# Kernel optimization log

Hardware: AMD Instinct MI355X
Metric: run time of the kernel (lower is better)

The kernel has to match this reference:

```python
import jax, jax.numpy as jnp
import numpy as np

B, S, HID = 4, 2048, 1024
H, D = 16, 64  # num_attention_heads, attention_head_size


def setup_inputs() -> dict:
    key = jax.random.key(0)
    k1, k2, k3, k4 = jax.random.split(key, 4)
    scale = 0.02
    return {
        "hidden_states": jax.random.normal(k1, (B, S, HID), dtype=jnp.float32),
        "attention_mask": jnp.zeros((B, 1, 1, S), dtype=jnp.float32),
        "Wq": jax.random.normal(k2, (HID, HID), dtype=jnp.float32) * scale,
        "bq": jnp.zeros((HID,), dtype=jnp.float32),
        "Wk": jax.random.normal(k3, (HID, HID), dtype=jnp.float32) * scale,
        "bk": jnp.zeros((HID,), dtype=jnp.float32),
        "Wv": jax.random.normal(k4, (HID, HID), dtype=jnp.float32) * scale,
        "bv": jnp.zeros((HID,), dtype=jnp.float32),
    }


def _split_heads(x):
    # [B,S,HID] -> [B,H,S,D]
    b, s, _ = x.shape
    return x.reshape(b, s, H, D).transpose(0, 2, 1, 3)


def reference(hidden_states, attention_mask, Wq, bq, Wk, bk, Wv, bv):
    # nn.Linear applies x @ W.T + b
    q = _split_heads(hidden_states @ Wq.T + bq)  # [B,H,S,D]
    k = _split_heads(hidden_states @ Wk.T + bk)
    v = _split_heads(hidden_states @ Wv.T + bv)
    scores = jnp.einsum("bhqd,bhkd->bhqk", q, k) / jnp.sqrt(jnp.float32(D))
    scores = scores + attention_mask  # additive mask, broadcast [B,1,1,S]
    probs = jax.nn.softmax(scores, axis=-1)  # dropout prob = 0 -> identity
    ctx = jnp.einsum("bhqk,bhkd->bhqd", probs, v)  # [B,H,S,D]
    ctx = ctx.transpose(0, 2, 1, 3).reshape(hidden_states.shape[0], hidden_states.shape[1], HID)
    return ctx
```

## Files before the change

kernel.cpp:

```cpp
#include <hip/hip_runtime.h>
#include <stdint.h>

#define BB 4
#define SS 2048
#define HID 1024
#define NH 16
#define DH 64

using bf16x8 = __attribute__((ext_vector_type(8))) short;
using f32x4  = __attribute__((ext_vector_type(4))) float;

#define LOG2E 1.44269504088896340736f

__device__ __forceinline__ ushort f2bf(float f) {
  union { float f; uint32_t u; } v; v.f = f;
  return (ushort)((v.u + 0x7FFFu + ((v.u >> 16) & 1u)) >> 16);
}

__device__ __forceinline__ uint32_t cvt_pk_bf16(float a, float b) {
  uint32_t r;
  asm("v_cvt_pk_bf16_f32 %0, %1, %2" : "=v"(r) : "v"(a), "v"(b));
  return r;
}

__device__ __forceinline__ float exp2_hw(float x) {
  float r;
  asm("v_exp_f32 %0, %1" : "=v"(r) : "v"(x));
  return r;
}

__device__ __forceinline__ void gload_lds16(const ushort* g, ushort* l) {
  __builtin_amdgcn_global_load_lds(
      (const __attribute__((address_space(1))) uint32_t*)g,
      (__attribute__((address_space(3))) uint32_t*)l, 16, 0, 0);
}

__device__ __forceinline__ int vperm(int j) {
  return (j & 0x23) | ((j & 0x0C) << 1) | ((j & 0x10) >> 2);
}

__global__ void cvt_kernel(const float* __restrict__ x, const float* __restrict__ wq,
                           const float* __restrict__ wk, const float* __restrict__ wv,
                           const float* __restrict__ am,
                           ushort* __restrict__ xbf, ushort* __restrict__ wbf,
                           float* __restrict__ maskL) {
  const int64_t NX4 = (int64_t)BB * SS * HID / 4;
  const int64_t NW4 = (int64_t)HID * HID / 4;
  const int64_t NWT = 3 * NW4;
  int64_t i = (int64_t)blockIdx.x * blockDim.x + threadIdx.x;
  if (i >= NX4 + NWT) {
    const int64_t jm = i - (NX4 + NWT);
    float4 v = ((const float4*)am)[jm];
    v.x *= LOG2E; v.y *= LOG2E; v.z *= LOG2E; v.w *= LOG2E;
    ((float4*)maskL)[jm] = v;
    return;
  }
  float4 v;
  ushort4* dst;
  if (i < NX4) {
    v = ((const float4*)x)[i];
    dst = (ushort4*)xbf + i;
  } else {
    int64_t j = i - NX4;
    int w = (int)(j >> 18);
    int64_t k = j & (NW4 - 1);
    const float* src = (w == 0) ? wq : (w == 1) ? wk : wv;
    v = ((const float4*)src)[k];
    dst = (ushort4*)wbf + j;
  }
  ushort4 o;
  o.x = f2bf(v.x); o.y = f2bf(v.y); o.z = f2bf(v.z); o.w = f2bf(v.w);
  *dst = o;
}

__global__ __launch_bounds__(512, 2) void qkv_gemm(
    const ushort* __restrict__ xbf, const ushort* __restrict__ wbf,
    const float* __restrict__ bq, const float* __restrict__ bk,
    const float* __restrict__ bv,
    ushort* __restrict__ qws, ushort* __restrict__ kws, ushort* __restrict__ vtws) {
  __shared__ short Al[2][256][64];
  __shared__ short Bl[2][192][64];

  const int tid = threadIdx.x, wid = tid >> 6, lane = tid & 63;
  const int colL = lane & 15, rowg = lane >> 4;
  const int wr = wid >> 2, wc = wid & 3;

  const int wgid = (blockIdx.x & 7) * 64 + (blockIdx.x >> 3);
  const int m0 = (wgid >> 4) * 256;
  const int n0 = (wgid & 15) * 192;

  const int swzcol = (((tid & 7) * 16) ^ (((tid >> 3) & 7) << 4)) >> 1;
  const ushort* aSrc = xbf + (int64_t)(m0 + (tid >> 3)) * HID + swzcol;
  const ushort* bSrc = wbf + (int64_t)(n0 + (tid >> 3)) * HID + swzcol;
  ushort* Al_u = (ushort*)&Al[0][0][0];
  ushort* Bl_u = (ushort*)&Bl[0][0][0];

  auto stageA = [&](int kt, int r, int ps) {
    gload_lds16(aSrc + r * 64 * HID + kt * 64, Al_u + ps * 16384 + r * 4096 + wid * 512);
  };
  auto stageB = [&](int kt, int r, int ps) {
    gload_lds16(bSrc + r * 64 * HID + kt * 64, Bl_u + ps * 12288 + r * 4096 + wid * 512);
  };

  const int xsw = (colL & 7) << 4;
  const int offk0 = (rowg * 16) ^ xsw;
  const int offk1 = (64 + rowg * 16) ^ xsw;
  const int arow = (wr * 128 + colL) * 128;
  const int brow = (wc * 48 + colL) * 128;
  const char* AlC = (const char*)&Al[0][0][0];
  const char* BlC = (const char*)&Bl[0][0][0];

  f32x4 acc[8][3];
#pragma unroll
  for (int i = 0; i < 8; ++i)
#pragma unroll
    for (int j = 0; j < 3; ++j)
#pragma unroll
      for (int r = 0; r < 4; ++r) acc[i][j][r] = 0.f;

  stageB(0, 0, 0); stageB(0, 1, 0); stageB(0, 2, 0);
  stageA(0, 0, 0); stageA(0, 2, 0); stageA(0, 1, 0); stageA(0, 3, 0);
  asm volatile("s_waitcnt vmcnt(2)" ::: "memory");
  __builtin_amdgcn_s_barrier();

#define DO_PHASE(P, S1, S2, PRE_BAR2)                                          \
  {                                                                            \
    const int mfa = 2 * (P), mfb = 2 * (P) + 1;                                \
    bf16x8 aA0 = *(const bf16x8*)(kA0 + mfa * 2048);                           \
    bf16x8 aA1 = *(const bf16x8*)(kA1 + mfa * 2048);                           \
    bf16x8 aB0 = *(const bf16x8*)(kA0 + mfb * 2048);                           \
    bf16x8 aB1 = *(const bf16x8*)(kA1 + mfb * 2048);                           \
    S1; S2;                                                                    \
    __builtin_amdgcn_s_barrier();                                              \
    __builtin_amdgcn_s_setprio(1);                                             \
    _Pragma("unroll")                                                          \
    for (int nf = 0; nf < 3; ++nf) {                                           \
      acc[mfa][nf] = __builtin_amdgcn_mfma_f32_16x16x32_bf16(aA0, bfr[nf][0], acc[mfa][nf], 0, 0, 0); \
      acc[mfa][nf] = __builtin_amdgcn_mfma_f32_16x16x32_bf16(aA1, bfr[nf][1], acc[mfa][nf], 0, 0, 0); \
      acc[mfb][nf] = __builtin_amdgcn_mfma_f32_16x16x32_bf16(aB0, bfr[nf][0], acc[mfb][nf], 0, 0, 0); \
      acc[mfb][nf] = __builtin_amdgcn_mfma_f32_16x16x32_bf16(aB1, bfr[nf][1], acc[mfb][nf], 0, 0, 0); \
    }                                                                          \
    __builtin_amdgcn_s_setprio(0);                                             \
    PRE_BAR2;                                                                  \
    __builtin_amdgcn_s_barrier();                                              \
  }

  for (int t = 0; t < 16; ++t) {
    const int p = t & 1;
    const int ps = p ^ 1;
    const bool st = (t < 15);
    const int kt = t + 1;
    const char* kA0 = AlC + p * 32768 + arow + offk0;
    const char* kA1 = AlC + p * 32768 + arow + offk1;
    const char* kB0 = BlC + p * 24576 + brow + offk0;
    const char* kB1 = BlC + p * 24576 + brow + offk1;

    bf16x8 bfr[3][2];
#pragma unroll
    for (int nf = 0; nf < 3; ++nf) {
      bfr[nf][0] = *(const bf16x8*)(kB0 + nf * 2048);
      bfr[nf][1] = *(const bf16x8*)(kB1 + nf * 2048);
    }

    DO_PHASE(0, if (st) stageB(kt, 0, ps), if (st) stageB(kt, 1, ps), )
    DO_PHASE(1, if (st) stageB(kt, 2, ps), if (st) stageA(kt, 0, ps),
             if (t == 15) { asm volatile("s_waitcnt vmcnt(0)" ::: "memory"); }
             else        { asm volatile("s_waitcnt vmcnt(4)" ::: "memory"); })
    DO_PHASE(2, if (st) stageA(kt, 2, ps), if (st) stageA(kt, 1, ps), )
    DO_PHASE(3, if (st) stageA(kt, 3, ps), ,
             if (t == 14) { asm volatile("s_waitcnt vmcnt(0)" ::: "memory"); }
             else if (st) { asm volatile("s_waitcnt vmcnt(2)" ::: "memory"); })
  }
#undef DO_PHASE

#pragma unroll
  for (int nf = 0; nf < 3; ++nf) {
    const int n = n0 + wc * 48 + nf * 16 + colL;
    const int which = n >> 10;
    const int c = n & 1023;
    const int h = c >> 6, d = c & 63;
    const float bias = ((which == 0) ? bq : (which == 1) ? bk : bv)[c];
#pragma unroll
    for (int mf = 0; mf < 8; ++mf) {
      const int mb = m0 + wr * 128 + mf * 16 + rowg * 4;
      const int b = mb >> 11, s = mb & 2047;
      const int bh = b * NH + h;
      if (which == 2) {
        ushort4 o;
        o.x = f2bf(acc[mf][nf][0] + bias);
        o.y = f2bf(acc[mf][nf][1] + bias);
        o.z = f2bf(acc[mf][nf][2] + bias);
        o.w = f2bf(acc[mf][nf][3] + bias);
        const int scol2 = (s & ~63) | vperm(s & 63);
        *(ushort4*)&vtws[((int64_t)bh * DH + d) * SS + scol2] = o;
      } else {
        ushort* dst = (which == 0) ? qws : kws;
#pragma unroll
        for (int r = 0; r < 4; ++r)
          dst[((int64_t)bh * SS + s + r) * DH + d] = f2bf(acc[mf][nf][r] + bias);
      }
    }
  }
}

__global__ __launch_bounds__(256, 3) void attn_kernel(
    const ushort* __restrict__ qws, const ushort* __restrict__ kws,
    const ushort* __restrict__ vtws, const float* __restrict__ maskL,
    float* __restrict__ out) {
  __shared__ short Kl[2][64][64];
  __shared__ short Vl[2][64][64];
  __shared__ float Ml[2048];

  const int tid = threadIdx.x, wid = tid >> 6, lane = tid & 63;
  const int bh = blockIdx.x, qb = blockIdx.y;
  const int b = bh >> 4, h = bh & 15;
  const int64_t qkb = (int64_t)bh * SS * DH;
  const int64_t vb  = (int64_t)bh * DH * SS;
  const int q0 = qb * 128;
  const int colL = lane & 15, rowg = lane >> 4;
  const float SCL = 0.125f * LOG2E;

  const int srow = wid * 16 + (lane >> 3);
  const int swzc = (((lane & 7) * 16) ^ ((lane >> 3) << 4)) >> 1;
  const ushort* gk = kws + qkb + (int64_t)srow * DH + swzc;
  const ushort* gv = vtws + vb + (int64_t)srow * SS + swzc;
  ushort* ldsK = (ushort*)&Kl[0][0][0] + wid * 1024;
  ushort* ldsV = (ushort*)&Vl[0][0][0] + wid * 1024;

  auto stageK = [&](int slot, int tt) {
    const ushort* k0 = gk + tt * 4096;
    gload_lds16(k0,       ldsK + slot * 4096);
    gload_lds16(k0 + 512, ldsK + slot * 4096 + 512);
  };
  auto stageV = [&](int slot, int tt) {
    const ushort* v0 = gv + tt * 64;
    gload_lds16(v0,          ldsV + slot * 4096);
    gload_lds16(v0 + 8 * SS, ldsV + slot * 4096 + 512);
  };
  auto stageMask = [&]() {
    const float* src = maskL + b * SS + (wid * 2) * 256 + lane * 4;
    gload_lds16((const ushort*)src,         (ushort*)(Ml + wid * 2 * 256));
    gload_lds16((const ushort*)(src + 256), (ushort*)(Ml + wid * 2 * 256 + 256));
  };

  const int xsw = (colL & 7) << 4;
  const char* kb0 = (const char*)&Kl[0][0][0] + colL * 128 + ((rowg * 16) ^ xsw);
  const char* kb1 = (const char*)&Kl[0][0][0] + colL * 128 + ((64 + rowg * 16) ^ xsw);
  const char* vb0 = (const char*)&Vl[0][0][0] + colL * 128 + ((rowg * 16) ^ xsw);
  const char* vb1 = (const char*)&Vl[0][0][0] + colL * 128 + ((64 + rowg * 16) ^ xsw);

  bf16x8 qf[2][2];
#pragma unroll
  for (int qh = 0; qh < 2; ++qh) {
    const ushort* gq = qws + qkb + (int64_t)(q0 + wid * 32 + qh * 16 + colL) * DH + rowg * 8;
    qf[qh][0] = *(const bf16x8*)(gq);
    qf[qh][1] = *(const bf16x8*)(gq + 32);
  }

  const f32x4 FZERO = {0.f, 0.f, 0.f, 0.f};
  union OU { uint32_t u[4]; bf16x8 v; } onesu;
  onesu.u[0] = 0x3F803F80u; onesu.u[1] = 0x3F803F80u;
  onesu.u[2] = 0x3F803F80u; onesu.u[3] = 0x3F803F80u;
  const bf16x8 ONES = onesu.v;

  f32x4 accO[2][4];
  f32x4 accL[2];
#pragma unroll
  for (int qh = 0; qh < 2; ++qh) {
    accL[qh] = FZERO;
#pragma unroll
    for (int dt = 0; dt < 4; ++dt)
#pragma unroll
      for (int r = 0; r < 4; ++r) accO[qh][dt][r] = 0.f;
  }

  f32x4 scA[2][4], scB[2][4];
  bf16x8 paf[2][2];

  auto qk = [&](int cur, f32x4 (&sc)[2][4]) {
    __builtin_amdgcn_s_setprio(1);
#pragma unroll
    for (int kt = 0; kt < 4; ++kt) {
      bf16x8 kf0 = *(const bf16x8*)(kb0 + cur * 8192 + kt * 2048);
      bf16x8 kf1 = *(const bf16x8*)(kb1 + cur * 8192 + kt * 2048);
      sc[0][kt] = __builtin_amdgcn_mfma_f32_16x16x32_bf16(kf0, qf[0][0], FZERO, 0, 0, 0);
      sc[0][kt] = __builtin_amdgcn_mfma_f32_16x16x32_bf16(kf1, qf[0][1], sc[0][kt], 0, 0, 0);
      sc[1][kt] = __builtin_amdgcn_mfma_f32_16x16x32_bf16(kf0, qf[1][0], FZERO, 0, 0, 0);
      sc[1][kt] = __builtin_amdgcn_mfma_f32_16x16x32_bf16(kf1, qf[1][1], sc[1][kt], 0, 0, 0);
    }
    __builtin_amdgcn_s_setprio(0);
  };

  auto soft = [&](int tm, f32x4 (&sc)[2][4]) {
    float4 m4[4];
#pragma unroll
    for (int kt = 0; kt < 4; ++kt)
      m4[kt] = *(const float4*)&Ml[tm * 64 + kt * 16 + rowg * 4];
#pragma unroll
    for (int qh = 0; qh < 2; ++qh) {
#pragma unroll
      for (int kt = 0; kt < 4; ++kt) {
        sc[qh][kt][0] = exp2_hw(fmaf(sc[qh][kt][0], SCL, m4[kt].x));
        sc[qh][kt][1] = exp2_hw(fmaf(sc[qh][kt][1], SCL, m4[kt].y));
        sc[qh][kt][2] = exp2_hw(fmaf(sc[qh][kt][2], SCL, m4[kt].z));
        sc[qh][kt][3] = exp2_hw(fmaf(sc[qh][kt][3], SCL, m4[kt].w));
      }
      union PU { uint32_t u[4]; bf16x8 v; } p0, p1;
      p0.u[0] = cvt_pk_bf16(sc[qh][0][0], sc[qh][0][1]);
      p0.u[1] = cvt_pk_bf16(sc[qh][0][2], sc[qh][0][3]);
      p0.u[2] = cvt_pk_bf16(sc[qh][1][0], sc[qh][1][1]);
      p0.u[3] = cvt_pk_bf16(sc[qh][1][2], sc[qh][1][3]);
      p1.u[0] = cvt_pk_bf16(sc[qh][2][0], sc[qh][2][1]);
      p1.u[1] = cvt_pk_bf16(sc[qh][2][2], sc[qh][2][3]);
      p1.u[2] = cvt_pk_bf16(sc[qh][3][0], sc[qh][3][1]);
      p1.u[3] = cvt_pk_bf16(sc[qh][3][2], sc[qh][3][3]);
      paf[qh][0] = p0.v;
      paf[qh][1] = p1.v;
    }
  };

  auto pv = [&](int slot) {
    __builtin_amdgcn_s_setprio(1);
#pragma unroll
    for (int ks = 0; ks < 2; ++ks) {
      accL[0] = __builtin_amdgcn_mfma_f32_16x16x32_bf16(paf[0][ks], ONES, accL[0], 0, 0, 0);
      accL[1] = __builtin_amdgcn_mfma_f32_16x16x32_bf16(paf[1][ks], ONES, accL[1], 0, 0, 0);
#pragma unroll
      for (int dt = 0; dt < 4; ++dt) {
        bf16x8 vf = *(const bf16x8*)((ks == 0 ? vb0 : vb1) + slot * 8192 + dt * 2048);
        accO[0][dt] = __builtin_amdgcn_mfma_f32_16x16x32_bf16(paf[0][ks], vf, accO[0][dt], 0, 0, 0);
        accO[1][dt] = __builtin_amdgcn_mfma_f32_16x16x32_bf16(paf[1][ks], vf, accO[1][dt], 0, 0, 0);
      }
    }
    __builtin_amdgcn_s_setprio(0);
  };

  auto fullstep = [&](int t, f32x4 (&scN)[2][4], f32x4 (&scO)[2][4],
                      bool stg, bool dopv) {
    const int cur = t & 1, prv = cur ^ 1;
    if (stg) stageK(prv, t + 1);
    qk(cur, scN);
    if (dopv) {
      soft(t - 1, scO);
      pv(prv);
    }
    __builtin_amdgcn_sched_barrier(0);
    __builtin_amdgcn_s_barrier();
    __builtin_amdgcn_sched_barrier(0);
    if (stg) {
      stageV(prv, t + 1);
      __builtin_amdgcn_sched_barrier(0);
      asm volatile("s_waitcnt vmcnt(2)" ::: "memory");
    } else {
      asm volatile("s_waitcnt vmcnt(0)" ::: "memory");
    }
    __builtin_amdgcn_s_barrier();
    __builtin_amdgcn_sched_barrier(0);
  };

  stageMask();
  stageK(0, 0);
  stageV(0, 0);
  asm volatile("s_waitcnt vmcnt(2)" ::: "memory");
  __builtin_amdgcn_s_barrier();
  __builtin_amdgcn_sched_barrier(0);

  fullstep(0, scA, scB, true, false);
  for (int t = 1; t < 31; t += 2) {
    fullstep(t,     scB, scA, true, true);
    fullstep(t + 1, scA, scB, true, true);
  }
  fullstep(31, scB, scA, false, true);

  soft(31, scB);
  pv(1);

#pragma unroll
  for (int qh = 0; qh < 2; ++qh) {
    float inv[4];
#pragma unroll
    for (int r = 0; r < 4; ++r) inv[r] = 1.0f / accL[qh][r];
#pragma unroll
    for (int dt = 0; dt < 4; ++dt)
#pragma unroll
      for (int r = 0; r < 4; ++r) {
        const int s = q0 + wid * 32 + qh * 16 + rowg * 4 + r;
        out[((int64_t)b * SS + s) * HID + h * DH + dt * 16 + colL] = accO[qh][dt][r] * inv[r];
      }
  }
}

extern "C" void kernel_launch(void* const* d_in, const int* in_sizes, int n_in,
                              void* d_out, int out_size, void* d_ws, size_t ws_size,
                              hipStream_t stream) {
  const float* x  = (const float*)d_in[0];
  const float* am = (const float*)d_in[1];
  const float* wq = (const float*)d_in[2];
  const float* bq = (const float*)d_in[3];
  const float* wk = (const float*)d_in[4];
  const float* bk = (const float*)d_in[5];
  const float* wv = (const float*)d_in[6];
  const float* bv = (const float*)d_in[7];
  float* out = (float*)d_out;
  char* ws = (char*)d_ws;

  ushort* xbf  = (ushort*)(ws);
  ushort* wbf  = (ushort*)(ws + 16777216);
  ushort* qws  = (ushort*)(ws + 23068672);
  ushort* kws  = (ushort*)(ws + 39845888);
  ushort* vtws = (ushort*)(ws + 56623104);
  float*  mskL = (float*)(ws + 73400320);

  hipLaunchKernelGGL(cvt_kernel, dim3(11272), dim3(256), 0, stream,
                     x, wq, wk, wv, am, xbf, wbf, mskL);
  hipLaunchKernelGGL(qkv_gemm, dim3(512), dim3(512), 0, stream,
                     xbf, wbf, bq, bk, bv, qws, kws, vtws);
  hipLaunchKernelGGL(attn_kernel, dim3(64, 16), dim3(256), 0, stream,
                     qws, kws, vtws, mskL, out);
}
```

Before: 160.5 us.

## Replace software-pipelined QK/PV schedule with simple loop and raise occupancy

Removes the two-stage software pipeline in which the QK of tile t overlapped the softmax and PV of tile t-1, and replaces it with a straightforward per-tile loop that prefetches both K and V for the next tile up front. Launch bounds go from 3 to 4 blocks per CU, so fewer live score registers are expected to let more waves hide latency. In exchange, intra-wave overlap of MFMA and exp work is lost, and the vmcnt waits and barriers are rearranged, which is risky for LDS correctness if the counts are off.

```diff
diff --git a/kernel.cpp b/kernel.cpp
--- a/kernel.cpp
+++ b/kernel.cpp
@@ -203,7 +203,7 @@
   }
 }
 
-__global__ __launch_bounds__(256, 3) void attn_kernel(
+__global__ __launch_bounds__(256, 4) void attn_kernel(
     const ushort* __restrict__ qws, const ushort* __restrict__ kws,
     const ushort* __restrict__ vtws, const float* __restrict__ maskL,
     float* __restrict__ out) {
@@ -274,10 +274,18 @@
       for (int r = 0; r < 4; ++r) accO[qh][dt][r] = 0.f;
   }
 
-  f32x4 scA[2][4], scB[2][4];
-  bf16x8 paf[2][2];
-
-  auto qk = [&](int cur, f32x4 (&sc)[2][4]) {
+  stageMask();
+  stageK(0, 0);
+  stageV(0, 0);
+  asm volatile("s_waitcnt vmcnt(2)" ::: "memory");
+  __builtin_amdgcn_s_barrier();
+
+  for (int t = 0; t < 32; ++t) {
+    const int cur = t & 1;
+    const bool st = (t < 31);
+    if (st) { stageK(cur ^ 1, t + 1); stageV(cur ^ 1, t + 1); }
+
+    f32x4 sc[2][4];
     __builtin_amdgcn_s_setprio(1);
 #pragma unroll
     for (int kt = 0; kt < 4; ++kt) {
@@ -289,13 +297,13 @@
       sc[1][kt] = __builtin_amdgcn_mfma_f32_16x16x32_bf16(kf1, qf[1][1], sc[1][kt], 0, 0, 0);
     }
     __builtin_amdgcn_s_setprio(0);
-  };
-
-  auto soft = [&](int tm, f32x4 (&sc)[2][4]) {
+
     float4 m4[4];
 #pragma unroll
     for (int kt = 0; kt < 4; ++kt)
-      m4[kt] = *(const float4*)&Ml[tm * 64 + kt * 16 + rowg * 4];
+      m4[kt] = *(const float4*)&Ml[t * 64 + kt * 16 + rowg * 4];
+
+    bf16x8 paf[2][2];
 #pragma unroll
     for (int qh = 0; qh < 2; ++qh) {
 #pragma unroll
@@ -317,9 +325,11 @@
       paf[qh][0] = p0.v;
       paf[qh][1] = p1.v;
     }
-  };
-
-  auto pv = [&](int slot) {
+
+    if (st) { asm volatile("s_waitcnt vmcnt(4)" ::: "memory"); }
+    else    { asm volatile("s_waitcnt vmcnt(0)" ::: "memory"); }
+    __builtin_amdgcn_s_barrier();
+
     __builtin_amdgcn_s_setprio(1);
 #pragma unroll
     for (int ks = 0; ks < 2; ++ks) {
@@ -327,53 +337,18 @@
       accL[1] = __builtin_amdgcn_mfma_f32_16x16x32_bf16(paf[1][ks], ONES, accL[1], 0, 0, 0);
 #pragma unroll
       for (int dt = 0; dt < 4; ++dt) {
-        bf16x8 vf = *(const bf16x8*)((ks == 0 ? vb0 : vb1) + slot * 8192 + dt * 2048);
+        bf16x8 vf = *(const bf16x8*)((ks == 0 ? vb0 : vb1) + cur * 8192 + dt * 2048);
         accO[0][dt] = __builtin_amdgcn_mfma_f32_16x16x32_bf16(paf[0][ks], vf, accO[0][dt], 0, 0, 0);
         accO[1][dt] = __builtin_amdgcn_mfma_f32_16x16x32_bf16(paf[1][ks], vf, accO[1][dt], 0, 0, 0);
       }
     }
     __builtin_amdgcn_s_setprio(0);
-  };
-
-  auto fullstep = [&](int t, f32x4 (&scN)[2][4], f32x4 (&scO)[2][4],
-                      bool stg, bool dopv) {
-    const int cur = t & 1, prv = cur ^ 1;
-    if (stg) stageK(prv, t + 1);
-    qk(cur, scN);
-    if (dopv) {
-      soft(t - 1, scO);
-      pv(prv);
-    }
-    __builtin_amdgcn_sched_barrier(0);
-    __builtin_amdgcn_s_barrier();
-    __builtin_amdgcn_sched_barrier(0);
-    if (stg) {
-      stageV(prv, t + 1);
-      __builtin_amdgcn_sched_barrier(0);
+
+    if (st) {
       asm volatile("s_waitcnt vmcnt(2)" ::: "memory");
-    } else {
-      asm volatile("s_waitcnt vmcnt(0)" ::: "memory");
-    }
-    __builtin_amdgcn_s_barrier();
-    __builtin_amdgcn_sched_barrier(0);
-  };
-
-  stageMask();
-  stageK(0, 0);
-  stageV(0, 0);
-  asm volatile("s_waitcnt vmcnt(2)" ::: "memory");
-  __builtin_amdgcn_s_barrier();
-  __builtin_amdgcn_sched_barrier(0);
-
-  fullstep(0, scA, scB, true, false);
-  for (int t = 1; t < 31; t += 2) {
-    fullstep(t,     scB, scA, true, true);
-    fullstep(t + 1, scA, scB, true, true);
-  }
-  fullstep(31, scB, scA, false, true);
-
-  soft(31, scB);
-  pv(1);
+      __builtin_amdgcn_s_barrier();
+    }
+  }
 
 #pragma unroll
   for (int qh = 0; qh < 2; ++qh) {
```

Result: faster. 152.8 us (-4.8%).
